# Kernel optimization log

Measured on AMD Instinct MI355X. Metric: run time of the kernel, lower is better.

## Reference

```python
import jax, jax.numpy as jnp
import numpy as np

N = 10000   # num nodes
E = 160000  # num edges (avg degree 16)
B = 8       # batch dim carried on node state
D = 64      # hidden_size


def setup_inputs() -> dict:
    key = jax.random.key(0)
    k1, k2, k3, k4, k5, k6 = jax.random.split(key, 6)
    state = jax.random.normal(k1, (N, B, D), jnp.float32)
    feature = jax.random.normal(k2, (N, 32), jnp.float32)  # unused by GAT math, kept for call signature
    weight = jax.random.normal(k3, (2 * D, D), jnp.float32) * 0.05
    src = jax.random.randint(k4, (E,), 0, N, jnp.int32)
    dst = jax.random.randint(k5, (E,), 0, N, jnp.int32)
    dist = jax.random.uniform(k6, (E, 1), jnp.float32)
    return dict(state=state, feature=feature, weight=weight, src=src, dst=dst, dist=dist)


def reference(state, feature, weight, src, dst, dist):
    # --- msg_edge: gather src/dst node states per edge ---
    src_state = state[src]                 # [E,B,D]
    dst_state = state[dst]                 # [E,B,D]
    es = jnp.concatenate([src_state, dst_state], axis=-1)          # [E,B,2D]
    alpha = jax.nn.leaky_relu(jnp.einsum('ebk,kd->ebd', es, weight),
                              negative_slope=0.2)                  # tf.nn.leaky_relu alpha=0.2
    alpha = alpha * dist[:, :, None]       # dist [E,1] broadcast to [E,1,1]

    # --- msg_reduce: segment softmax over incoming edges of each dst node ---
    amax = jax.ops.segment_max(alpha, dst, num_segments=N)         # [N,B,D]
    ex = jnp.exp(alpha - amax[dst])                                # stable exp
    denom = jax.ops.segment_sum(ex, dst, num_segments=N)           # [N,B,D]
    attn = ex / denom[dst]                                         # [E,B,D]

    # weighted sum of src states scattered back to dst nodes, then relu
    new_state = jax.nn.relu(jax.ops.segment_sum(attn * src_state, dst, num_segments=N))
    return new_state
```

## Files before the change

kernel.cpp:

```cpp
#include <hip/hip_runtime.h>
#include <hip/hip_fp16.h>
#include <math.h>

#define N_NODES 10000
#define N_EDGES 160000
#define B_ 8
#define D_ 64
#define BD 512
#define ROWS 80000
#define SLICE 640000
#define CAP 48
#define CAPR 56

typedef _Float16 f16x8 __attribute__((ext_vector_type(8)));
typedef float f32x4 __attribute__((ext_vector_type(4)));
typedef float f4v __attribute__((ext_vector_type(4)));
typedef unsigned int u32;

union HU { _Float16 f; unsigned short u; };
union HC { u32 u; __half2 h; };

__global__ void __launch_bounds__(256, 4) prep_kernel(
    const int* __restrict__ src, const int* __restrict__ dst,
    const float* __restrict__ dist, int* __restrict__ counts, u32* __restrict__ bucket,
    const float* __restrict__ state, const float* __restrict__ weight,
    u32* __restrict__ G, __half* __restrict__ Pd) {
    __shared__ _Float16 At[64 * 72];
    __shared__ char smemB[128 * 72 * 2];
    _Float16* Bt = (_Float16*)smemB;
    unsigned short* Ps2 = (unsigned short*)smemB;
    unsigned short* Ps  = (unsigned short*)(smemB + 8704);
    int bid = blockIdx.x;
    int tid = threadIdx.x;

    int s_e, d_e; float di_e;
    bool do_edge = tid < 128;
    if (do_edge) {
        int e = bid * 128 + tid;
        s_e = src[e];
        d_e = dst[e];
        di_e = dist[e];
    }

    int row0 = bid * 64;
    int wave = tid >> 6, lane = tid & 63;
    int quad = lane >> 4, m16 = lane & 15;
    int m_loc = wave * 16 + m16;

    const f4v* st4 = (const f4v*)(state + (size_t)row0 * 64);
    for (int i = tid; i < 1024; i += 256) {
        int r = i >> 4, c4 = (i & 15) << 2;
        f4v v = __builtin_nontemporal_load(&st4[i]);
        union { short4 s; _Float16 h[4]; } u;
        u.h[0] = (_Float16)v[0]; u.h[1] = (_Float16)v[1];
        u.h[2] = (_Float16)v[2]; u.h[3] = (_Float16)v[3];
        *(short4*)&At[r * 72 + c4] = u.s;
    }
    const f4v* w4 = (const f4v*)weight;
    for (int i = tid; i < 2048; i += 256) {
        int r = i >> 4, c4 = (i & 15) << 2;
        f4v v = w4[i];
        int h = r >> 6, k = r & 63;
        int nb = h * 64 + c4;
        Bt[(nb + 0) * 72 + k] = (_Float16)v[0];
        Bt[(nb + 1) * 72 + k] = (_Float16)v[1];
        Bt[(nb + 2) * 72 + k] = (_Float16)v[2];
        Bt[(nb + 3) * 72 + k] = (_Float16)v[3];
    }

    if (do_edge) {
        int pos = atomicAdd(&counts[d_e], 1);
        if (pos < CAP) {
            unsigned short hd = __half_as_ushort(__float2half_rn(di_e * 1.44269504f));
            bucket[d_e * CAPR + pos] = (u32)s_e | ((u32)hd << 16);
        }
    }
    __syncthreads();

    f16x8 bf0[8], bf1[8];
#pragma unroll
    for (int tcol = 0; tcol < 8; tcol++) {
        int n = tcol * 16 + m16;
        bf0[tcol] = *(const f16x8*)&Bt[n * 72 + quad * 8];
        bf1[tcol] = *(const f16x8*)&Bt[n * 72 + 32 + quad * 8];
    }
    f16x8 a0 = *(const f16x8*)&At[m_loc * 72 + quad * 8];
    f16x8 a1 = *(const f16x8*)&At[m_loc * 72 + 32 + quad * 8];
    __syncthreads();

#pragma unroll
    for (int tcol = 0; tcol < 8; tcol++) {
        int n = tcol * 16 + m16;
        f32x4 acc = {0.f, 0.f, 0.f, 0.f};
        acc = __builtin_amdgcn_mfma_f32_16x16x32_f16(a0, bf0[tcol], acc, 0, 0, 0);
        acc = __builtin_amdgcn_mfma_f32_16x16x32_f16(a1, bf1[tcol], acc, 0, 0, 0);
#pragma unroll
        for (int r = 0; r < 4; r++) {
            int ml = wave * 16 + quad * 4 + r;
            unsigned short ph = __half_as_ushort(__float2half_rn(acc[r]));
            if (tcol < 4) Ps2[ml * 68 + n] = ph;
            else          Ps[ml * 64 + (n - 64)] = ph;
        }
    }
    __syncthreads();

    const u32* Ps2w = (const u32*)Ps2;
    const u32* Atw = (const u32*)At;
    for (int i = tid; i < 1024; i += 256) {
        int row = i >> 4, q = i & 15;
        int m = row0 + row;
        size_t base = (size_t)(m & 7) * SLICE + (size_t)(m >> 3) * 64;
        u32 p01 = Ps2w[row * 34 + q * 2];
        u32 p23 = Ps2w[row * 34 + q * 2 + 1];
        u32 x01 = Atw[row * 36 + q * 2];
        u32 x23 = Atw[row * 36 + q * 2 + 1];
        float4 v = make_float4(__uint_as_float(p01), __uint_as_float(p23),
                               __uint_as_float(x01), __uint_as_float(x23));
        *(float4*)&G[base + q * 4] = v;
    }
    for (int i = tid; i < 512; i += 256) {
        int row = i >> 3, seg = i & 7;
        int m = row0 + row;
        size_t base = (size_t)(m & 7) * SLICE + (size_t)(m >> 3) * 64;
        *(float4*)&Pd[base + seg * 8] = *(const float4*)&Ps[row * 64 + seg * 8];
    }
}

__global__ void __launch_bounds__(256) gat_aggregate(
    const u32* __restrict__ G,
    const __half* __restrict__ Pds,
    const int* __restrict__ counts,
    const u32* __restrict__ bucket,
    float* __restrict__ out) {
    int bid = blockIdx.x;
    int b = bid & 7;
    int grp = bid >> 3;
    int wave = threadIdx.x >> 6;
    int lane = threadIdx.x & 63;
    int n0 = (grp << 3) + (wave << 1);
    int n1 = n0 + 1;
    int eidx = lane >> 4;
    int lpart = lane & 15;

    const u32* Gb = G + (size_t)b * SLICE;
    const __half* Pb = Pds + (size_t)b * SLICE;

    int2 c01 = *(const int2*)(counts + n0);
    int cnt0 = c01.x > CAP ? CAP : c01.x;
    int cnt1 = c01.y > CAP ? CAP : c01.y;
    const u32* ep0 = bucket + n0 * CAPR;
    const u32* ep1 = bucket + n1 * CAPR;

    union { double d; __half2 h[2]; } pdu0, pdu1;
    pdu0.d = *(const double*)(Pb + n0 * 64 + lpart * 4);
    pdu1.d = *(const double*)(Pb + n1 * 64 + lpart * 4);

    u32 rA0 = ep0[eidx], rB0 = ep0[4 + eidx];
    u32 rA1 = ep1[eidx], rB1 = ep1[4 + eidx];
    float4 gA0 = *(const float4*)(Gb + (size_t)(rA0 & 0xffffu) * 64 + lpart * 4);
    float4 gB0 = *(const float4*)(Gb + (size_t)(rB0 & 0xffffu) * 64 + lpart * 4);
    float4 gA1 = *(const float4*)(Gb + (size_t)(rA1 & 0xffffu) * 64 + lpart * 4);
    float4 gB1 = *(const float4*)(Gb + (size_t)(rB1 & 0xffffu) * 64 + lpart * 4);
    __half hh;
    hh = __ushort_as_half((unsigned short)(rA0 >> 16)); __half2 dA0 = __halves2half2(hh, hh);
    hh = __ushort_as_half((unsigned short)(rB0 >> 16)); __half2 dB0 = __halves2half2(hh, hh);
    hh = __ushort_as_half((unsigned short)(rA1 >> 16)); __half2 dA1 = __halves2half2(hh, hh);
    hh = __ushort_as_half((unsigned short)(rB1 >> 16)); __half2 dB1 = __halves2half2(hh, hh);

    const __half2 c06 = __float2half2_rn(0.6f);
    const __half2 c04 = __float2half2_rn(0.4f);

    auto edge_body = [&](float4 g, __half2 dd, __half2 pd01, __half2 pd23,
                         __half2& l01, __half2& l23, __half2& o01, __half2& o23) {
        union { float4 f; __half2 h[4]; } gu; gu.f = g;
        __half2 z01 = __hadd2(gu.h[0], pd01);
        __half2 z23 = __hadd2(gu.h[1], pd23);
        HC zz01, zz23, az01, az23;
        zz01.h = z01; zz23.h = z23;
        az01.u = zz01.u & 0x7fff7fffu;
        az23.u = zz23.u & 0x7fff7fffu;
        __half2 lk01 = __hfma2(az01.h, c04, __hmul2(z01, c06));
        __half2 lk23 = __hfma2(az23.h, c04, __hmul2(z23, c06));
        __half2 a01 = __hmul2(lk01, dd);
        __half2 a23 = __hmul2(lk23, dd);
        __half2 e01 = __halves2half2(hexp2(__low2half(a01)), hexp2(__high2half(a01)));
        __half2 e23 = __halves2half2(hexp2(__low2half(a23)), hexp2(__high2half(a23)));
        l01 = __hadd2(l01, e01);
        l23 = __hadd2(l23, e23);
        o01 = __hfma2(e01, gu.h[2], o01);
        o23 = __hfma2(e23, gu.h[3], o23);
    };

    auto run_task = [&](const u32* ep, int cnt, __half2 pd01, __half2 pd23,
                        float4 ga, float4 gb, __half2 da, __half2 db,
                        __half2& l01, __half2& l23, __half2& o01, __half2& o23) {
        int Gn = ((cnt + 3) & ~3) >> 2;
        if (Gn <= 0) return;
        u32 rq = 0;
        if (Gn > 2) rq = ep[8 + eidx];
        for (int g = 0; g < Gn; ++g) {
            u32 rn = 0;
            if (g + 3 < Gn) rn = ep[4 * (g + 3) + eidx];
            float4 gn; __half2 dn;
            bool have_n = (g + 2 < Gn);
            if (have_n) {
                gn = *(const float4*)(Gb + (size_t)(rq & 0xffffu) * 64 + lpart * 4);
                __half hd = __ushort_as_half((unsigned short)(rq >> 16));
                dn = __halves2half2(hd, hd);
            }
            edge_body(ga, da, pd01, pd23, l01, l23, o01, o23);
            ga = gb; da = db;
            if (have_n) { gb = gn; db = dn; }
            rq = rn;
        }
    };

    __half2 zero = __float2half2_rn(0.f);
    __half2 l01a = zero, l23a = zero, o01a = zero, o23a = zero;
    __half2 l01b = zero, l23b = zero, o01b = zero, o23b = zero;

    run_task(ep0, cnt0, pdu0.h[0], pdu0.h[1], gA0, gB0, dA0, dB0, l01a, l23a, o01a, o23a);
    run_task(ep1, cnt1, pdu1.h[0], pdu1.h[1], gA1, gB1, dA1, dB1, l01b, l23b, o01b, o23b);

    float4 g0 = *(const float4*)(Gb + lpart * 4);
    union { float4 f; __half2 h[4]; } g0u; g0u.f = g0;

    auto finish = [&](int cnt, __half2& l01, __half2& l23, __half2& o01, __half2& o23) {
        if (cnt <= 0) return;
#pragma unroll
        for (int m = 16; m <= 32; m <<= 1) {
            HC c;
            c.u = (u32)__shfl_xor((int)((HC){.h = l01}).u, m, 64); l01 = __hadd2(l01, c.h);
            c.u = (u32)__shfl_xor((int)((HC){.h = l23}).u, m, 64); l23 = __hadd2(l23, c.h);
            c.u = (u32)__shfl_xor((int)((HC){.h = o01}).u, m, 64); o01 = __hadd2(o01, c.h);
            c.u = (u32)__shfl_xor((int)((HC){.h = o23}).u, m, 64); o23 = __hadd2(o23, c.h);
        }
        int npads = ((cnt + 3) & ~3) - cnt;
        if (npads) {
            __half2 np = __float2half2_rn((float)npads);
            l01 = __hsub2(l01, np);
            l23 = __hsub2(l23, np);
            __half2 nneg = __hneg2(np);
            o01 = __hfma2(nneg, g0u.h[2], o01);
            o23 = __hfma2(nneg, g0u.h[3], o23);
        }
    };
    finish(cnt0, l01a, l23a, o01a, o23a);
    finish(cnt1, l01b, l23b, o01b, o23b);

    if (eidx == 0) {
        auto emit = [&](int n, int cnt, __half2 l01, __half2 l23, __half2 o01, __half2 o23) {
            float4 r;
            if (cnt > 0) {
                float l0 = __low2float(l01), l1 = __high2float(l01);
                float l2 = __low2float(l23), l3 = __high2float(l23);
                float o0 = __low2float(o01), o1 = __high2float(o01);
                float o2 = __low2float(o23), o3 = __high2float(o23);
                r.x = fmaxf(o0 * __builtin_amdgcn_rcpf(l0), 0.f);
                r.y = fmaxf(o1 * __builtin_amdgcn_rcpf(l1), 0.f);
                r.z = fmaxf(o2 * __builtin_amdgcn_rcpf(l2), 0.f);
                r.w = fmaxf(o3 * __builtin_amdgcn_rcpf(l3), 0.f);
            } else {
                r = make_float4(0.f, 0.f, 0.f, 0.f);
            }
            *(float4*)(out + (size_t)n * BD + b * 64 + lpart * 4) = r;
        };
        emit(n0, cnt0, l01a, l23a, o01a, o23a);
        emit(n1, cnt1, l01b, l23b, o01b, o23b);
    }
}

extern "C" void kernel_launch(void* const* d_in, const int* in_sizes, int n_in,
                              void* d_out, int out_size, void* d_ws, size_t ws_size,
                              hipStream_t stream) {
    const float* state  = (const float*)d_in[0];
    const float* weight = (const float*)d_in[2];
    const int*   src    = (const int*)d_in[3];
    const int*   dst    = (const int*)d_in[4];
    const float* dist   = (const float*)d_in[5];

    u32*    G      = (u32*)d_ws;
    __half* Pd     = (__half*)(G + (size_t)8 * SLICE);
    u32*    bucket = (u32*)(Pd + (size_t)8 * SLICE);
    int*    counts = (int*)(bucket + (size_t)N_NODES * CAPR);

    hipMemsetAsync(bucket, 0, ((size_t)N_NODES * CAPR + N_NODES) * sizeof(u32), stream);
    prep_kernel<<<1250, 256, 0, stream>>>(src, dst, dist, counts, bucket,
                                          state, weight, G, Pd);
    gat_aggregate<<<N_NODES, 256, 0, stream>>>(G, Pd, counts, bucket, (float*)d_out);
}
```

Measured before the change: 141.3 us.

## Switch G/Pd to node-major layout and process one node per wave

The intermediate G and Pd buffers move from batch-sliced layout to node-major [N][B][64], so each gathered edge row is one contiguous 2 KB block. The aggregate kernel now gives one wave a whole node across all 8 batches and walks edges sequentially two at a time. This replaces the old split of four edge groups across lanes and removes the shuffle reduction and padding correction. It loses the old software prefetch pipeline, and each wave now serially iterates all edges of its node.

```diff
diff --git a/kernel.cpp b/kernel.cpp
--- a/kernel.cpp
+++ b/kernel.cpp
@@ -7,8 +7,6 @@
 #define B_ 8
 #define D_ 64
 #define BD 512
-#define ROWS 80000
-#define SLICE 640000
 #define CAP 48
 #define CAPR 56
 
@@ -109,7 +107,7 @@
     for (int i = tid; i < 1024; i += 256) {
         int row = i >> 4, q = i & 15;
         int m = row0 + row;
-        size_t base = (size_t)(m & 7) * SLICE + (size_t)(m >> 3) * 64;
+        size_t base = (size_t)(m >> 3) * 512 + (size_t)(m & 7) * 64;
         u32 p01 = Ps2w[row * 34 + q * 2];
         u32 p23 = Ps2w[row * 34 + q * 2 + 1];
         u32 x01 = Atw[row * 36 + q * 2];
@@ -121,7 +119,7 @@
     for (int i = tid; i < 512; i += 256) {
         int row = i >> 3, seg = i & 7;
         int m = row0 + row;
-        size_t base = (size_t)(m & 7) * SLICE + (size_t)(m >> 3) * 64;
+        size_t base = (size_t)(m >> 3) * 512 + (size_t)(m & 7) * 64;
         *(float4*)&Pd[base + seg * 8] = *(const float4*)&Ps[row * 64 + seg * 8];
     }
 }
@@ -132,142 +130,81 @@
     const int* __restrict__ counts,
     const u32* __restrict__ bucket,
     float* __restrict__ out) {
-    int bid = blockIdx.x;
-    int b = bid & 7;
-    int grp = bid >> 3;
     int wave = threadIdx.x >> 6;
     int lane = threadIdx.x & 63;
-    int n0 = (grp << 3) + (wave << 1);
-    int n1 = n0 + 1;
-    int eidx = lane >> 4;
-    int lpart = lane & 15;
-
-    const u32* Gb = G + (size_t)b * SLICE;
-    const __half* Pb = Pds + (size_t)b * SLICE;
-
-    int2 c01 = *(const int2*)(counts + n0);
-    int cnt0 = c01.x > CAP ? CAP : c01.x;
-    int cnt1 = c01.y > CAP ? CAP : c01.y;
-    const u32* ep0 = bucket + n0 * CAPR;
-    const u32* ep1 = bucket + n1 * CAPR;
-
-    union { double d; __half2 h[2]; } pdu0, pdu1;
-    pdu0.d = *(const double*)(Pb + n0 * 64 + lpart * 4);
-    pdu1.d = *(const double*)(Pb + n1 * 64 + lpart * 4);
-
-    u32 rA0 = ep0[eidx], rB0 = ep0[4 + eidx];
-    u32 rA1 = ep1[eidx], rB1 = ep1[4 + eidx];
-    float4 gA0 = *(const float4*)(Gb + (size_t)(rA0 & 0xffffu) * 64 + lpart * 4);
-    float4 gB0 = *(const float4*)(Gb + (size_t)(rB0 & 0xffffu) * 64 + lpart * 4);
-    float4 gA1 = *(const float4*)(Gb + (size_t)(rA1 & 0xffffu) * 64 + lpart * 4);
-    float4 gB1 = *(const float4*)(Gb + (size_t)(rB1 & 0xffffu) * 64 + lpart * 4);
-    __half hh;
-    hh = __ushort_as_half((unsigned short)(rA0 >> 16)); __half2 dA0 = __halves2half2(hh, hh);
-    hh = __ushort_as_half((unsigned short)(rB0 >> 16)); __half2 dB0 = __halves2half2(hh, hh);
-    hh = __ushort_as_half((unsigned short)(rA1 >> 16)); __half2 dA1 = __halves2half2(hh, hh);
-    hh = __ushort_as_half((unsigned short)(rB1 >> 16)); __half2 dB1 = __halves2half2(hh, hh);
+    int n = (blockIdx.x << 2) + wave;
+
+    int offA = lane * 4;
+    int offB = offA + 256;
+
+    int cnt = counts[n]; if (cnt > CAP) cnt = CAP;
+    const u32* ep = bucket + n * CAPR;
+
+    union { double d; __half2 h[2]; } pdA, pdB;
+    pdA.d = *(const double*)(Pds + (size_t)n * 512 + offA);
+    pdB.d = *(const double*)(Pds + (size_t)n * 512 + offB);
 
     const __half2 c06 = __float2half2_rn(0.6f);
     const __half2 c04 = __float2half2_rn(0.4f);
-
-    auto edge_body = [&](float4 g, __half2 dd, __half2 pd01, __half2 pd23,
-                         __half2& l01, __half2& l23, __half2& o01, __half2& o23) {
-        union { float4 f; __half2 h[4]; } gu; gu.f = g;
-        __half2 z01 = __hadd2(gu.h[0], pd01);
-        __half2 z23 = __hadd2(gu.h[1], pd23);
-        HC zz01, zz23, az01, az23;
-        zz01.h = z01; zz23.h = z23;
-        az01.u = zz01.u & 0x7fff7fffu;
-        az23.u = zz23.u & 0x7fff7fffu;
-        __half2 lk01 = __hfma2(az01.h, c04, __hmul2(z01, c06));
-        __half2 lk23 = __hfma2(az23.h, c04, __hmul2(z23, c06));
-        __half2 a01 = __hmul2(lk01, dd);
-        __half2 a23 = __hmul2(lk23, dd);
-        __half2 e01 = __halves2half2(hexp2(__low2half(a01)), hexp2(__high2half(a01)));
-        __half2 e23 = __halves2half2(hexp2(__low2half(a23)), hexp2(__high2half(a23)));
-        l01 = __hadd2(l01, e01);
-        l23 = __hadd2(l23, e23);
-        o01 = __hfma2(e01, gu.h[2], o01);
-        o23 = __hfma2(e23, gu.h[3], o23);
+    __half2 zero = __float2half2_rn(0.f);
+    __half2 lA0 = zero, lA1 = zero, oA0 = zero, oA1 = zero;
+    __half2 lB0 = zero, lB1 = zero, oB0 = zero, oB1 = zero;
+
+    auto lrexp = [&](__half2 z, __half2 dd) -> __half2 {
+        HC zz, az; zz.h = z;
+        az.u = zz.u & 0x7fff7fffu;
+        __half2 lk = __hfma2(az.h, c04, __hmul2(z, c06));
+        __half2 aa = __hmul2(lk, dd);
+        return __halves2half2(hexp2(__low2half(aa)), hexp2(__high2half(aa)));
     };
 
-    auto run_task = [&](const u32* ep, int cnt, __half2 pd01, __half2 pd23,
-                        float4 ga, float4 gb, __half2 da, __half2 db,
-                        __half2& l01, __half2& l23, __half2& o01, __half2& o23) {
-        int Gn = ((cnt + 3) & ~3) >> 2;
-        if (Gn <= 0) return;
-        u32 rq = 0;
-        if (Gn > 2) rq = ep[8 + eidx];
-        for (int g = 0; g < Gn; ++g) {
-            u32 rn = 0;
-            if (g + 3 < Gn) rn = ep[4 * (g + 3) + eidx];
-            float4 gn; __half2 dn;
-            bool have_n = (g + 2 < Gn);
-            if (have_n) {
-                gn = *(const float4*)(Gb + (size_t)(rq & 0xffffu) * 64 + lpart * 4);
-                __half hd = __ushort_as_half((unsigned short)(rq >> 16));
-                dn = __halves2half2(hd, hd);
-            }
-            edge_body(ga, da, pd01, pd23, l01, l23, o01, o23);
-            ga = gb; da = db;
-            if (have_n) { gb = gn; db = dn; }
-            rq = rn;
-        }
+    auto body = [&](float4 g1, float4 g2, __half2 dd) {
+        union { float4 f; __half2 h[4]; } u1, u2; u1.f = g1; u2.f = g2;
+        __half2 e;
+        e = lrexp(__hadd2(u1.h[0], pdA.h[0]), dd); lA0 = __hadd2(lA0, e); oA0 = __hfma2(e, u1.h[2], oA0);
+        e = lrexp(__hadd2(u1.h[1], pdA.h[1]), dd); lA1 = __hadd2(lA1, e); oA1 = __hfma2(e, u1.h[3], oA1);
+        e = lrexp(__hadd2(u2.h[0], pdB.h[0]), dd); lB0 = __hadd2(lB0, e); oB0 = __hfma2(e, u2.h[2], oB0);
+        e = lrexp(__hadd2(u2.h[1], pdB.h[1]), dd); lB1 = __hadd2(lB1, e); oB1 = __hfma2(e, u2.h[3], oB1);
     };
 
-    __half2 zero = __float2half2_rn(0.f);
-    __half2 l01a = zero, l23a = zero, o01a = zero, o23a = zero;
-    __half2 l01b = zero, l23b = zero, o01b = zero, o23b = zero;
-
-    run_task(ep0, cnt0, pdu0.h[0], pdu0.h[1], gA0, gB0, dA0, dB0, l01a, l23a, o01a, o23a);
-    run_task(ep1, cnt1, pdu1.h[0], pdu1.h[1], gA1, gB1, dA1, dB1, l01b, l23b, o01b, o23b);
-
-    float4 g0 = *(const float4*)(Gb + lpart * 4);
-    union { float4 f; __half2 h[4]; } g0u; g0u.f = g0;
-
-    auto finish = [&](int cnt, __half2& l01, __half2& l23, __half2& o01, __half2& o23) {
-        if (cnt <= 0) return;
-#pragma unroll
-        for (int m = 16; m <= 32; m <<= 1) {
-            HC c;
-            c.u = (u32)__shfl_xor((int)((HC){.h = l01}).u, m, 64); l01 = __hadd2(l01, c.h);
-            c.u = (u32)__shfl_xor((int)((HC){.h = l23}).u, m, 64); l23 = __hadd2(l23, c.h);
-            c.u = (u32)__shfl_xor((int)((HC){.h = o01}).u, m, 64); o01 = __hadd2(o01, c.h);
-            c.u = (u32)__shfl_xor((int)((HC){.h = o23}).u, m, 64); o23 = __hadd2(o23, c.h);
-        }
-        int npads = ((cnt + 3) & ~3) - cnt;
-        if (npads) {
-            __half2 np = __float2half2_rn((float)npads);
-            l01 = __hsub2(l01, np);
-            l23 = __hsub2(l23, np);
-            __half2 nneg = __hneg2(np);
-            o01 = __hfma2(nneg, g0u.h[2], o01);
-            o23 = __hfma2(nneg, g0u.h[3], o23);
-        }
-    };
-    finish(cnt0, l01a, l23a, o01a, o23a);
-    finish(cnt1, l01b, l23b, o01b, o23b);
-
-    if (eidx == 0) {
-        auto emit = [&](int n, int cnt, __half2 l01, __half2 l23, __half2 o01, __half2 o23) {
-            float4 r;
-            if (cnt > 0) {
-                float l0 = __low2float(l01), l1 = __high2float(l01);
-                float l2 = __low2float(l23), l3 = __high2float(l23);
-                float o0 = __low2float(o01), o1 = __high2float(o01);
-                float o2 = __low2float(o23), o3 = __high2float(o23);
-                r.x = fmaxf(o0 * __builtin_amdgcn_rcpf(l0), 0.f);
-                r.y = fmaxf(o1 * __builtin_amdgcn_rcpf(l1), 0.f);
-                r.z = fmaxf(o2 * __builtin_amdgcn_rcpf(l2), 0.f);
-                r.w = fmaxf(o3 * __builtin_amdgcn_rcpf(l3), 0.f);
-            } else {
-                r = make_float4(0.f, 0.f, 0.f, 0.f);
-            }
-            *(float4*)(out + (size_t)n * BD + b * 64 + lpart * 4) = r;
-        };
-        emit(n0, cnt0, l01a, l23a, o01a, o23a);
-        emit(n1, cnt1, l01b, l23b, o01b, o23b);
-    }
+    for (int j = 0; j < cnt; j += 2) {
+        u32 ra = ep[j];
+        bool two = (j + 1) < cnt;
+        u32 rb = two ? ep[j + 1] : 0u;
+        const u32* pa = G + (size_t)(ra & 0xffffu) * 512;
+        float4 ga1 = *(const float4*)(pa + offA);
+        float4 ga2 = *(const float4*)(pa + offB);
+        float4 gb1, gb2;
+        if (two) {
+            const u32* pb = G + (size_t)(rb & 0xffffu) * 512;
+            gb1 = *(const float4*)(pb + offA);
+            gb2 = *(const float4*)(pb + offB);
+        }
+        __half ha = __ushort_as_half((unsigned short)(ra >> 16));
+        body(ga1, ga2, __halves2half2(ha, ha));
+        if (two) {
+            __half hb = __ushort_as_half((unsigned short)(rb >> 16));
+            body(gb1, gb2, __halves2half2(hb, hb));
+        }
+    }
+
+    float* op = out + (size_t)n * BD;
+    float4 rA, rB;
+    if (cnt > 0) {
+        rA.x = fmaxf(__low2float(oA0)  * __builtin_amdgcn_rcpf(__low2float(lA0)),  0.f);
+        rA.y = fmaxf(__high2float(oA0) * __builtin_amdgcn_rcpf(__high2float(lA0)), 0.f);
+        rA.z = fmaxf(__low2float(oA1)  * __builtin_amdgcn_rcpf(__low2float(lA1)),  0.f);
+        rA.w = fmaxf(__high2float(oA1) * __builtin_amdgcn_rcpf(__high2float(lA1)), 0.f);
+        rB.x = fmaxf(__low2float(oB0)  * __builtin_amdgcn_rcpf(__low2float(lB0)),  0.f);
+        rB.y = fmaxf(__high2float(oB0) * __builtin_amdgcn_rcpf(__high2float(lB0)), 0.f);
+        rB.z = fmaxf(__low2float(oB1)  * __builtin_amdgcn_rcpf(__low2float(lB1)),  0.f);
+        rB.w = fmaxf(__high2float(oB1) * __builtin_amdgcn_rcpf(__high2float(lB1)), 0.f);
+    } else {
+        rA = make_float4(0.f, 0.f, 0.f, 0.f);
+        rB = rA;
+    }
+    *(float4*)(op + offA) = rA;
+    *(float4*)(op + offB) = rB;
 }
 
 extern "C" void kernel_launch(void* const* d_in, const int* in_sizes, int n_in,
@@ -280,12 +217,12 @@
     const float* dist   = (const float*)d_in[5];
 
     u32*    G      = (u32*)d_ws;
-    __half* Pd     = (__half*)(G + (size_t)8 * SLICE);
-    u32*    bucket = (u32*)(Pd + (size_t)8 * SLICE);
+    __half* Pd     = (__half*)(G + (size_t)N_NODES * 512);
+    u32*    bucket = (u32*)(Pd + (size_t)N_NODES * 512);
     int*    counts = (int*)(bucket + (size_t)N_NODES * CAPR);
 
     hipMemsetAsync(bucket, 0, ((size_t)N_NODES * CAPR + N_NODES) * sizeof(u32), stream);
     prep_kernel<<<1250, 256, 0, stream>>>(src, dst, dist, counts, bucket,
                                           state, weight, G, Pd);
-    gat_aggregate<<<N_NODES, 256, 0, stream>>>(G, Pd, counts, bucket, (float*)d_out);
+    gat_aggregate<<<2500, 256, 0, stream>>>(G, Pd, counts, bucket, (float*)d_out);
 }
```

New measurement: 146.2 us. +3.5%, slower.
